# Performance work log

Measured on AMD Instinct MI355X. Metric: run time of the kernel, lower is better.

The kernel has to match this reference:

```python
import jax, jax.numpy as jnp
import numpy as np

D_MODEL = 1024
D_FF = 4096
N_EXPERTS = 8
TOP_K = 2

def setup_inputs() -> dict:
    key = jax.random.key(0)
    ks = jax.random.split(key, 6)
    s = lambda fan_in: 1.0 / np.sqrt(fan_in)
    x = jax.random.normal(ks[0], (4, 2048, D_MODEL), dtype=jnp.float32)
    Wg = jax.random.normal(ks[1], (D_MODEL, N_EXPERTS), dtype=jnp.float32) * s(D_MODEL)
    W1 = jax.random.normal(ks[2], (N_EXPERTS, D_MODEL, D_FF), dtype=jnp.float32) * s(D_MODEL)
    b1 = jax.random.normal(ks[3], (N_EXPERTS, D_FF), dtype=jnp.float32) * 0.01
    W2 = jax.random.normal(ks[4], (N_EXPERTS, D_FF, D_MODEL), dtype=jnp.float32) * s(D_FF)
    b2 = jax.random.normal(ks[5], (N_EXPERTS, D_MODEL), dtype=jnp.float32) * 0.01
    return {"x": x, "Wg": Wg, "W1": W1, "b1": b1, "W2": W2, "b2": b2}

def reference(x, Wg, W1, b1, W2, b2):
    B, L, D = x.shape
    xf = x.reshape(B * L, D)               # (N, D)
    N = xf.shape[0]
    E = Wg.shape[1]
    # gating
    logits = xf @ Wg                        # (N, E)
    probs = jax.nn.softmax(logits, axis=-1)
    topv, topi = jax.lax.top_k(probs, TOP_K)          # (N, K)
    w = topv / (topv.sum(axis=-1, keepdims=True) + 1e-9)
    rows = jnp.arange(N)[:, None]
    combine = jnp.zeros((N, E), xf.dtype).at[rows, topi].set(w)    # (N, E) combine weights
    dispatch = jnp.zeros((N, E), xf.dtype).at[rows, topi].set(1.0)
    aux_loss = (dispatch.mean(axis=0) * probs.mean(axis=0)).sum() * E
    # experts: dense per-expert FFN, masked-combined (zero weight => zero contribution),
    # mathematically identical to the torch masked gather/scatter loop.
    out = jnp.zeros_like(xf)
    for e in range(E):  # fixed small loop over experts
        h = jax.nn.gelu(xf @ W1[e] + b1[e], approximate=False)   # (N, d_ff)
        out = out + combine[:, e:e + 1] * (h @ W2[e] + b2[e])
    return out.reshape(B, L, D), aux_loss
```

## Files before the change

kernel.cpp:

```cpp
#include <hip/hip_runtime.h>
#include <math.h>

#define D_MODEL 1024
#define D_FF    4096
#define NEXP    8
#define NTOK    8192
#define NASSIGN (NTOK*2)
#define NGBLK   (NTOK/4)

using short8 = __attribute__((ext_vector_type(8))) short;
using short4v = __attribute__((ext_vector_type(4))) short;
using f32x4  = __attribute__((ext_vector_type(4))) float;

__device__ __forceinline__ short f2bf(float f) {
  unsigned u = __float_as_uint(f);
  unsigned r = (u + 0x7fffu + ((u >> 16) & 1u)) >> 16;
  return (short)r;
}

__device__ __forceinline__ void gload_lds16(const void* g, void* l) {
  __builtin_amdgcn_global_load_lds((const __attribute__((address_space(1))) void*)g,
                                   (__attribute__((address_space(3))) void*)l, 16, 0, 0);
}

__device__ __forceinline__ float gelu_f(float x) {
  float z = 0.70710678118f * x;
  float a = fabsf(z);
  float t = 1.0f / (1.0f + 0.3275911f * a);
  float p = t * (0.254829592f + t * (-0.284496736f + t * (1.421413741f +
            t * (-1.453152027f + t * 1.061405429f))));
  float er = 1.0f - p * __expf(-a * a);
  er = copysignf(er, z);
  return 0.5f * x * (1.0f + er);
}

__global__ void zero_kernel(int* ctrl) {
  int i = threadIdx.x;
  if (i < 24) ctrl[i] = 0;
}

__global__ __launch_bounds__(256) void transpose_conv(const float* __restrict__ in, short* __restrict__ out,
                                                      int R, int C) {
  __shared__ float t[64][65];
  int e = blockIdx.z;
  size_t base = (size_t)e * R * C;
  int r0 = blockIdx.y * 64, c0 = blockIdx.x * 64;
  int lr = threadIdx.x >> 6, lc = threadIdx.x & 63;
#pragma unroll
  for (int j = 0; j < 16; ++j) {
    int rr = lr + j * 4;
    t[rr][lc] = in[base + (size_t)(r0 + rr) * C + c0 + lc];
  }
  __syncthreads();
#pragma unroll
  for (int j = 0; j < 16; ++j) {
    int oc = lr + j * 4;
    out[base + (size_t)(c0 + oc) * R + r0 + lc] = f2bf(t[lc][oc]);
  }
}

__global__ __launch_bounds__(256) void gating_kernel(const float* __restrict__ x, const float* __restrict__ Wg,
                                                     int* __restrict__ assign_e, float* __restrict__ assign_w,
                                                     int* __restrict__ cnt_part, float* __restrict__ psum_part,
                                                     ushort4* __restrict__ xb4) {
  __shared__ float l_ps[NEXP];
  __shared__ int   l_cnt[NEXP];
  int tid = threadIdx.x, wv = tid >> 6, lane = tid & 63;
  if (tid < NEXP) { l_ps[tid] = 0.f; l_cnt[tid] = 0; }
  __syncthreads();

  int t = blockIdx.x * 4 + wv;
  const float4* xr = (const float4*)(x + (size_t)t * D_MODEL);
  float acc[NEXP];
#pragma unroll
  for (int e = 0; e < NEXP; ++e) acc[e] = 0.f;
#pragma unroll
  for (int i = 0; i < 4; ++i) {
    int c4 = lane + 64 * i;
    float4 v = xr[c4];
    ushort4 o;
    o.x = (unsigned short)f2bf(v.x); o.y = (unsigned short)f2bf(v.y);
    o.z = (unsigned short)f2bf(v.z); o.w = (unsigned short)f2bf(v.w);
    xb4[(size_t)t * 256 + c4] = o;
    const float* wr = Wg + c4 * 4 * NEXP;
#pragma unroll
    for (int j = 0; j < 4; ++j) {
      float xv = (&v.x)[j];
#pragma unroll
      for (int e = 0; e < NEXP; ++e) acc[e] += xv * wr[j * NEXP + e];
    }
  }
#pragma unroll
  for (int off = 32; off; off >>= 1)
#pragma unroll
    for (int e = 0; e < NEXP; ++e) acc[e] += __shfl_down(acc[e], off);

  if (lane == 0) {
    float m = acc[0];
#pragma unroll
    for (int e = 1; e < NEXP; ++e) m = fmaxf(m, acc[e]);
    float p[NEXP], s = 0.f;
#pragma unroll
    for (int e = 0; e < NEXP; ++e) { p[e] = expf(acc[e] - m); s += p[e]; }
    float inv = 1.f / s;
#pragma unroll
    for (int e = 0; e < NEXP; ++e) p[e] *= inv;
    int i0 = 0; float v0 = p[0];
#pragma unroll
    for (int e = 1; e < NEXP; ++e) if (p[e] > v0) { v0 = p[e]; i0 = e; }
    int i1 = -1; float v1 = -1.f;
#pragma unroll
    for (int e = 0; e < NEXP; ++e) if (e != i0 && p[e] > v1) { v1 = p[e]; i1 = e; }
    float denom = 1.f / (v0 + v1 + 1e-9f);
    assign_e[2 * t] = i0;     assign_w[2 * t] = v0 * denom;
    assign_e[2 * t + 1] = i1; assign_w[2 * t + 1] = v1 * denom;
    atomicAdd(&l_cnt[i0], 1);
    atomicAdd(&l_cnt[i1], 1);
#pragma unroll
    for (int e = 0; e < NEXP; ++e) atomicAdd(&l_ps[e], p[e]);
  }
  __syncthreads();
  if (tid < NEXP) {
    psum_part[blockIdx.x * NEXP + tid] = l_ps[tid];
    cnt_part[blockIdx.x * NEXP + tid] = l_cnt[tid];
  }
}

__global__ __launch_bounds__(256) void scan_kernel(const int* __restrict__ cnt_part, const float* __restrict__ psum_part,
                                                   int* __restrict__ cnt, int* __restrict__ offs,
                                                   float* __restrict__ aux_out) {
  __shared__ float sp[256];
  __shared__ int   sc[256];
  int tid = threadIdx.x;
  int e = tid & 7, c = tid >> 3;
  float fs = 0.f; int is = 0;
  for (int b = c; b < NGBLK; b += 32) {
    fs += psum_part[b * NEXP + e];
    is += cnt_part[b * NEXP + e];
  }
  sp[tid] = fs; sc[tid] = is;
  __syncthreads();
  if (tid < NEXP) {
    float f = 0.f; int n = 0;
    for (int c2 = 0; c2 < 32; ++c2) { f += sp[c2 * 8 + tid]; n += sc[c2 * 8 + tid]; }
    cnt[tid] = n; sp[tid] = f;
  }
  __syncthreads();
  if (tid == 0) {
    int o = 0; float aux = 0.f;
    for (int e2 = 0; e2 < NEXP; ++e2) {
      offs[e2] = o; o += cnt[e2];
      aux += (float)cnt[e2] * sp[e2];
    }
    aux_out[0] = aux * (float)NEXP / ((float)NTOK * (float)NTOK);
  }
}

__global__ __launch_bounds__(256) void scatter_kernel(const int* __restrict__ assign_e,
                                                      const int* __restrict__ offs, int* __restrict__ cursor,
                                                      int* __restrict__ slot_tok, int* __restrict__ slot_of) {
  __shared__ int lhist[NEXP], lbase[NEXP];
  int tid = threadIdx.x;
  int a = blockIdx.x * 256 + tid;
  if (tid < NEXP) lhist[tid] = 0;
  __syncthreads();
  int e = assign_e[a];
  int lp = atomicAdd(&lhist[e], 1);
  __syncthreads();
  if (tid < NEXP) lbase[tid] = atomicAdd(&cursor[tid], lhist[tid]);
  __syncthreads();
  int s = offs[e] + lbase[e] + lp;
  slot_tok[s] = a >> 1;
  slot_of[a] = s;
}

template<int KD, int ND, int RT, int EPI>
__global__ __launch_bounds__(512, 2) void gemm8p(
    const short* __restrict__ Asrc, const short* __restrict__ Bsrc,
    const float* __restrict__ bias, const int* __restrict__ slot_tok,
    const int* __restrict__ cnt, const int* __restrict__ offs,
    void* __restrict__ OutP)
{
  constexpr int NT = KD / 64;
  constexpr int NP = ND / 256;
  extern __shared__ char ldsb[];

  int bid = blockIdx.x;
  int x = bid & 7, rr = bid >> 3;
  int ft = rr % NP, q0 = rr / NP;
  int g = q0 * 8 + x;
  int e = g / RT, rt = g % RT;
  int cn = cnt[e];
  if (rt * 256 >= cn) return;
  int off = offs[e];
  int tid = threadIdx.x, l = tid & 63, w = tid >> 6;
  int wm = w >> 2, wn = w & 3;
  int l15 = l & 15, kh = l >> 4;

  int srw = tid >> 3;
  int swz = ((tid & 7) ^ (srw & 7)) * 8;
  const short* ar[4];
  const short* br[4];
#pragma unroll
  for (int s = 0; s < 4; ++s) {
    int gr = rt * 256 + s * 64 + srw;
    int ic = gr < cn ? gr : cn - 1;
    if (EPI == 0) ar[s] = Asrc + (size_t)slot_tok[off + ic] * KD + swz;
    else          ar[s] = Asrc + (size_t)(off + ic) * KD + swz;
    br[s] = Bsrc + (size_t)e * ND * KD + (size_t)(ft * 256 + s * 64 + srw) * KD + swz;
  }

#define STAGE(P, TAU) do {                                                        \
    int _b = (TAU) & 1;                                                           \
    const short* _p0 = ((P) >= 2 ? ar : br)[(P) & 1];                             \
    const short* _p1 = ((P) >= 2 ? ar : br)[((P) & 1) + 2];                       \
    char* _d = ldsb + _b * 65536 + ((P) >= 2 ? 0 : 32768);                        \
    gload_lds16(_p0 + (size_t)(TAU) * 64, _d + ((P) & 1) * 8192 + tid * 16);      \
    gload_lds16(_p1 + (size_t)(TAU) * 64, _d + (((P) & 1) + 2) * 8192 + tid * 16);\
  } while (0)

  STAGE(0, 0); STAGE(1, 0); STAGE(2, 0); STAGE(3, 0);
  STAGE(0, 1);
  asm volatile("s_waitcnt vmcnt(2)" ::: "memory");
  asm volatile("s_barrier" ::: "memory");

  int cx0 = ((0 * 4 + kh) ^ (l15 & 7)) << 4;
  int cx1 = ((1 * 4 + kh) ^ (l15 & 7)) << 4;
  int arow = (wm * 128 + l15) << 7;
  int brow = (wn * 64 + l15) << 7;
  f32x4 acc[8][4] = {};
  short8 bq[4], af[4];

  for (int t = 0; t < NT; ++t) {
    const char* Ab = ldsb + (t & 1) * 65536;
    const char* Bb = Ab + 32768;
#pragma unroll
    for (int q = 0; q < 4; ++q) {
      const int kk = q >> 1, mh = q & 1;
      const int cx = kk ? cx1 : cx0;
      if (q == 0 || q == 2) {
#pragma unroll
        for (int n = 0; n < 4; ++n) bq[n] = *(const short8*)(Bb + brow + (n << 11) + cx);
      }
#pragma unroll
      for (int m = 0; m < 4; ++m) af[m] = *(const short8*)(Ab + arow + ((mh * 64 + m * 16) << 7) + cx);
      {
        int tpp = t + ((q + 5) >> 2);
        if (tpp < NT) STAGE((q + 1) & 3, tpp);
      }
      asm volatile("s_barrier" ::: "memory");
      __builtin_amdgcn_s_setprio(1);
#pragma unroll
      for (int m = 0; m < 4; ++m)
#pragma unroll
        for (int n = 0; n < 4; ++n)
          acc[mh * 4 + m][n] = __builtin_amdgcn_mfma_f32_16x16x32_bf16(bq[n], af[m], acc[mh * 4 + m][n], 0, 0, 0);
      __builtin_amdgcn_s_setprio(0);
      if (q == 3) {
        if (t < NT - 2)       { asm volatile("s_waitcnt vmcnt(2)" ::: "memory"); }
        else if (t == NT - 2) { asm volatile("s_waitcnt vmcnt(0)" ::: "memory"); }
      }
      asm volatile("s_barrier" ::: "memory");
    }
  }
#undef STAGE

  int ftb = ft * 256;
  f32x4 b4[4];
#pragma unroll
  for (int n = 0; n < 4; ++n) b4[n] = *(const f32x4*)&bias[e * ND + ftb + wn * 64 + n * 16 + kh * 4];

  if (EPI == 1) {
    float* Y = (float*)OutP;
#pragma unroll
    for (int mi = 0; mi < 8; ++mi) {
      int tok = rt * 256 + wm * 128 + mi * 16 + l15;
      if (tok < cn) {
#pragma unroll
        for (int n = 0; n < 4; ++n) {
          f32x4 o;
#pragma unroll
          for (int j = 0; j < 4; ++j) o[j] = acc[mi][n][j] + b4[n][j];
          *(f32x4*)&Y[(size_t)(off + tok) * ND + ftb + wn * 64 + n * 16 + kh * 4] = o;
        }
      }
    }
  } else {
    short* H = (short*)OutP;
    char* slab = ldsb + w * 2048;
#pragma unroll
    for (int mi = 0; mi < 8; ++mi) {
#pragma unroll
      for (int n = 0; n < 4; ++n) {
        short4v h;
#pragma unroll
        for (int j = 0; j < 4; ++j) h[j] = f2bf(gelu_f(acc[mi][n][j] + b4[n][j]));
        int chunk = n * 2 + (kh >> 1);
        *(short4v*)(slab + l15 * 128 + ((chunk ^ (l15 & 7)) << 4) + ((kh & 1) << 3)) = h;
      }
      int tr = l >> 2;
      int tok = rt * 256 + wm * 128 + mi * 16 + tr;
      if (tok < cn) {
#pragma unroll
        for (int cc = 0; cc < 2; ++cc) {
          int c2 = (l & 3) * 2 + cc;
          short8 v = *(const short8*)(slab + tr * 128 + ((c2 ^ (tr & 7)) << 4));
          *(short8*)&H[(size_t)(off + tok) * ND + ftb + wn * 64 + c2 * 8] = v;
        }
      }
      asm volatile("s_waitcnt lgkmcnt(0)" ::: "memory");
    }
  }
}

__global__ __launch_bounds__(256) void combine_kernel(const float* __restrict__ y, const int* __restrict__ slot_of,
                                                      const float* __restrict__ assign_w, float* __restrict__ out) {
  int t = blockIdx.x;
  int d4 = threadIdx.x;
  int s0 = slot_of[2 * t], s1 = slot_of[2 * t + 1];
  float w0 = assign_w[2 * t], w1 = assign_w[2 * t + 1];
  float4 a = ((const float4*)(y + (size_t)s0 * D_MODEL))[d4];
  float4 b = ((const float4*)(y + (size_t)s1 * D_MODEL))[d4];
  float4 o;
  o.x = w0 * a.x + w1 * b.x;
  o.y = w0 * a.y + w1 * b.y;
  o.z = w0 * a.z + w1 * b.z;
  o.w = w0 * a.w + w1 * b.w;
  ((float4*)(out + (size_t)t * D_MODEL))[d4] = o;
}

extern "C" void kernel_launch(void* const* d_in, const int* in_sizes, int n_in,
                              void* d_out, int out_size, void* d_ws, size_t ws_size,
                              hipStream_t stream) {
  const float* x  = (const float*)d_in[0];
  const float* Wg = (const float*)d_in[1];
  const float* W1 = (const float*)d_in[2];
  const float* b1 = (const float*)d_in[3];
  const float* W2 = (const float*)d_in[4];
  const float* b2 = (const float*)d_in[5];
  float* out = (float*)d_out;
  char* ws = (char*)d_ws;

  short* xb       = (short*)(ws);
  short* w1t      = (short*)(ws + 16777216);
  float* y        = (float*)(ws + 16777216);
  short* w2t      = (short*)(ws + 83886080);
  short* H        = (short*)(ws + 150994944);
  int*   slot_tok = (int*)  (ws + 285212672);
  int*   assign_e = (int*)  (ws + 285278208);
  float* assign_w = (float*)(ws + 285343744);
  int*   slot_of  = (int*)  (ws + 285409280);
  int*   cnt_part = (int*)  (ws + 285474816);
  float* psum_part= (float*)(ws + 285540352);
  int*   ctrl     = (int*)  (ws + 285605888);
  int* cnt = ctrl; int* cursor = ctrl + 8; int* offs = ctrl + 16;

  hipFuncSetAttribute(reinterpret_cast<const void*>(&gemm8p<D_MODEL, D_FF, 12, 0>),
                      hipFuncAttributeMaxDynamicSharedMemorySize, 131072);
  hipFuncSetAttribute(reinterpret_cast<const void*>(&gemm8p<D_FF, D_MODEL, 12, 1>),
                      hipFuncAttributeMaxDynamicSharedMemorySize, 131072);

  zero_kernel<<<1, 64, 0, stream>>>(ctrl);
  transpose_conv<<<dim3(64, 16, NEXP), 256, 0, stream>>>(W1, w1t, D_MODEL, D_FF);
  transpose_conv<<<dim3(16, 64, NEXP), 256, 0, stream>>>(W2, w2t, D_FF, D_MODEL);
  gating_kernel<<<NGBLK, 256, 0, stream>>>(x, Wg, assign_e, assign_w, cnt_part, psum_part,
                                           (ushort4*)xb);
  scan_kernel<<<1, 256, 0, stream>>>(cnt_part, psum_part, cnt, offs, out + (out_size - 1));
  scatter_kernel<<<NASSIGN / 256, 256, 0, stream>>>(assign_e, offs, cursor, slot_tok, slot_of);
  gemm8p<D_MODEL, D_FF, 12, 0><<<12 * (D_FF / 256) * 8, 512, 131072, stream>>>(
      xb, w1t, b1, slot_tok, cnt, offs, H);
  gemm8p<D_FF, D_MODEL, 12, 1><<<12 * (D_MODEL / 256) * 8, 512, 131072, stream>>>(
      H, w2t, b2, slot_tok, cnt, offs, y);
  combine_kernel<<<NTOK, 256, 0, stream>>>(y, slot_of, assign_w, out);
}
```

Baseline: 609.7 us.

## Remap GEMM blocks across experts and double-buffer fragment registers in K loop

Block indices are remapped so that the eight XCD-interleaved neighbours handle different experts via (x+k)&7, with ft derived from k. The goal is to balance load across chiplets and give better L2 reuse of weight tiles. The inner K loop is restructured with two register sets for the A and B fragments, so the next fragment reads are issued before the current MFMA group and LDS latency overlaps with matrix math. This raises VGPR pressure under launch_bounds(512,2), which could cause spills or changed scheduling.

After: 555.6 us. 1.1x faster.

```diff
diff --git a/kernel.cpp b/kernel.cpp
--- a/kernel.cpp
+++ b/kernel.cpp
@@ -186,10 +186,10 @@
   extern __shared__ char ldsb[];
 
   int bid = blockIdx.x;
-  int x = bid & 7, rr = bid >> 3;
-  int ft = rr % NP, q0 = rr / NP;
-  int g = q0 * 8 + x;
-  int e = g / RT, rt = g % RT;
+  int x = bid & 7, j = bid >> 3;
+  int k = j / RT, rt = j % RT;
+  int ft = k % NP;
+  int e = (x + k) & 7;
   int cn = cnt[e];
   if (rt * 256 >= cn) return;
   int off = offs[e];
@@ -229,39 +229,65 @@
   int arow = (wm * 128 + l15) << 7;
   int brow = (wn * 64 + l15) << 7;
   f32x4 acc[8][4] = {};
-  short8 bq[4], af[4];
+  short8 bqA[4], bqB[4], afA[4], afB[4];
 
   for (int t = 0; t < NT; ++t) {
     const char* Ab = ldsb + (t & 1) * 65536;
     const char* Bb = Ab + 32768;
 #pragma unroll
-    for (int q = 0; q < 4; ++q) {
-      const int kk = q >> 1, mh = q & 1;
-      const int cx = kk ? cx1 : cx0;
-      if (q == 0 || q == 2) {
-#pragma unroll
-        for (int n = 0; n < 4; ++n) bq[n] = *(const short8*)(Bb + brow + (n << 11) + cx);
-      }
-#pragma unroll
-      for (int m = 0; m < 4; ++m) af[m] = *(const short8*)(Ab + arow + ((mh * 64 + m * 16) << 7) + cx);
-      {
-        int tpp = t + ((q + 5) >> 2);
-        if (tpp < NT) STAGE((q + 1) & 3, tpp);
-      }
-      asm volatile("s_barrier" ::: "memory");
-      __builtin_amdgcn_s_setprio(1);
-#pragma unroll
-      for (int m = 0; m < 4; ++m)
-#pragma unroll
-        for (int n = 0; n < 4; ++n)
-          acc[mh * 4 + m][n] = __builtin_amdgcn_mfma_f32_16x16x32_bf16(bq[n], af[m], acc[mh * 4 + m][n], 0, 0, 0);
-      __builtin_amdgcn_s_setprio(0);
-      if (q == 3) {
-        if (t < NT - 2)       { asm volatile("s_waitcnt vmcnt(2)" ::: "memory"); }
-        else if (t == NT - 2) { asm volatile("s_waitcnt vmcnt(0)" ::: "memory"); }
-      }
-      asm volatile("s_barrier" ::: "memory");
-    }
+    for (int n = 0; n < 4; ++n) bqA[n] = *(const short8*)(Bb + brow + (n << 11) + cx0);
+#pragma unroll
+    for (int m = 0; m < 4; ++m) afA[m] = *(const short8*)(Ab + arow + ((m * 16) << 7) + cx0);
+    if (t + 1 < NT) STAGE(1, t + 1);
+#pragma unroll
+    for (int m = 0; m < 4; ++m) afB[m] = *(const short8*)(Ab + arow + ((64 + m * 16) << 7) + cx0);
+    asm volatile("s_barrier" ::: "memory");
+    __builtin_amdgcn_s_setprio(1);
+#pragma unroll
+    for (int m = 0; m < 4; ++m)
+#pragma unroll
+      for (int n = 0; n < 4; ++n)
+        acc[m][n] = __builtin_amdgcn_mfma_f32_16x16x32_bf16(bqA[n], afA[m], acc[m][n], 0, 0, 0);
+    __builtin_amdgcn_s_setprio(0);
+    asm volatile("s_barrier" ::: "memory");
+    if (t + 1 < NT) STAGE(2, t + 1);
+#pragma unroll
+    for (int m = 0; m < 4; ++m) afA[m] = *(const short8*)(Ab + arow + ((m * 16) << 7) + cx1);
+#pragma unroll
+    for (int n = 0; n < 4; ++n) bqB[n] = *(const short8*)(Bb + brow + (n << 11) + cx1);
+    asm volatile("s_barrier" ::: "memory");
+    __builtin_amdgcn_s_setprio(1);
+#pragma unroll
+    for (int m = 0; m < 4; ++m)
+#pragma unroll
+      for (int n = 0; n < 4; ++n)
+        acc[4 + m][n] = __builtin_amdgcn_mfma_f32_16x16x32_bf16(bqA[n], afB[m], acc[4 + m][n], 0, 0, 0);
+    __builtin_amdgcn_s_setprio(0);
+    asm volatile("s_barrier" ::: "memory");
+    if (t + 1 < NT) STAGE(3, t + 1);
+#pragma unroll
+    for (int m = 0; m < 4; ++m) afB[m] = *(const short8*)(Ab + arow + ((64 + m * 16) << 7) + cx1);
+    asm volatile("s_barrier" ::: "memory");
+    __builtin_amdgcn_s_setprio(1);
+#pragma unroll
+    for (int m = 0; m < 4; ++m)
+#pragma unroll
+      for (int n = 0; n < 4; ++n)
+        acc[m][n] = __builtin_amdgcn_mfma_f32_16x16x32_bf16(bqB[n], afA[m], acc[m][n], 0, 0, 0);
+    __builtin_amdgcn_s_setprio(0);
+    asm volatile("s_barrier" ::: "memory");
+    if (t + 2 < NT) STAGE(0, t + 2);
+    asm volatile("s_barrier" ::: "memory");
+    __builtin_amdgcn_s_setprio(1);
+#pragma unroll
+    for (int m = 0; m < 4; ++m)
+#pragma unroll
+      for (int n = 0; n < 4; ++n)
+        acc[4 + m][n] = __builtin_amdgcn_mfma_f32_16x16x32_bf16(bqB[n], afB[m], acc[4 + m][n], 0, 0, 0);
+    __builtin_amdgcn_s_setprio(0);
+    if (t < NT - 2)       { asm volatile("s_waitcnt vmcnt(2)" ::: "memory"); }
+    else if (t == NT - 2) { asm volatile("s_waitcnt vmcnt(0)" ::: "memory"); }
+    asm volatile("s_barrier" ::: "memory");
   }
 #undef STAGE
 
@@ -280,7 +306,7 @@
         for (int n = 0; n < 4; ++n) {
           f32x4 o;
 #pragma unroll
-          for (int j = 0; j < 4; ++j) o[j] = acc[mi][n][j] + b4[n][j];
+          for (int jj = 0; jj < 4; ++jj) o[jj] = acc[mi][n][jj] + b4[n][jj];
           *(f32x4*)&Y[(size_t)(off + tok) * ND + ftb + wn * 64 + n * 16 + kh * 4] = o;
         }
       }
@@ -294,7 +320,7 @@
       for (int n = 0; n < 4; ++n) {
         short4v h;
 #pragma unroll
-        for (int j = 0; j < 4; ++j) h[j] = f2bf(gelu_f(acc[mi][n][j] + b4[n][j]));
+        for (int jj = 0; jj < 4; ++jj) h[jj] = f2bf(gelu_f(acc[mi][n][jj] + b4[n][jj]));
         int chunk = n * 2 + (kh >> 1);
         *(short4v*)(slab + l15 * 128 + ((chunk ^ (l15 & 7)) << 4) + ((kh & 1) << 3)) = h;
       }
@@ -367,9 +393,9 @@
                                            (ushort4*)xb);
   scan_kernel<<<1, 256, 0, stream>>>(cnt_part, psum_part, cnt, offs, out + (out_size - 1));
   scatter_kernel<<<NASSIGN / 256, 256, 0, stream>>>(assign_e, offs, cursor, slot_tok, slot_of);
-  gemm8p<D_MODEL, D_FF, 12, 0><<<12 * (D_FF / 256) * 8, 512, 131072, stream>>>(
+  gemm8p<D_MODEL, D_FF, 12, 0><<<8 * 16 * 12, 512, 131072, stream>>>(
       xb, w1t, b1, slot_tok, cnt, offs, H);
-  gemm8p<D_FF, D_MODEL, 12, 1><<<12 * (D_MODEL / 256) * 8, 512, 131072, stream>>>(
+  gemm8p<D_FF, D_MODEL, 12, 1><<<8 * 4 * 12, 512, 131072, stream>>>(
       H, w2t, b2, slot_tok, cnt, offs, y);
   combine_kernel<<<NTOK, 256, 0, stream>>>(y, slot_of, assign_w, out);
 }
```
